# Kernel tuning notes

Hardware: AMD Instinct MI355X
Metric: run time of the kernel (lower is better)

The kernel has to match this reference:

```python
import jax, jax.numpy as jnp
import numpy as np

N = 50000
E = 640000
M = 400000
D_IN, H1, H2, H3, D_OUT = 256, 128, 128, 64, 32


def _glorot(key, shape, gain=1.0):
    fan_in, fan_out = shape[0], shape[1]
    lim = gain * np.sqrt(6.0 / (fan_in + fan_out))
    return jax.random.uniform(key, shape, jnp.float32, -lim, lim)


def setup_inputs() -> dict:
    key = jax.random.key(0)
    ks = jax.random.split(key, 16)
    x = jax.random.normal(ks[0], (N, D_IN), jnp.float32)
    edge_index = jax.random.randint(ks[1], (2, E), 0, N, jnp.int64)
    train_sample = jax.random.randint(ks[2], (M, 2), 0, N, jnp.int64)
    g = 1.414
    return {
        "x": x,
        "edge_index": edge_index,
        "train_sample": train_sample,
        "W1": _glorot(ks[3], (D_IN, H1)),
        "W2": _glorot(ks[4], (H1, H2)),
        "tf_w1": _glorot(ks[5], (H2, H3), g), "tf_b1": jnp.zeros((H3,), jnp.float32),
        "tf_w2": _glorot(ks[6], (H3, D_OUT), g), "tf_b2": jnp.zeros((D_OUT,), jnp.float32),
        "tg_w1": _glorot(ks[7], (H2, H3), g), "tg_b1": jnp.zeros((H3,), jnp.float32),
        "tg_w2": _glorot(ks[8], (H3, D_OUT), g), "tg_b2": jnp.zeros((D_OUT,), jnp.float32),
    }


def _gcn_conv(x, W, src, dst, norm, n):
    # GCNConv (no bias): out = D^-1/2 (A+I) D^-1/2 (x @ W)
    h = x @ W
    msg = h[src] * norm[:, None]          # [E+N, H]
    return jax.ops.segment_sum(msg, dst, num_segments=n)


def reference(x, edge_index, train_sample, W1, W2, tf_w1, tf_b1, tf_w2, tf_b2, tg_w1, tg_b1, tg_w2, tg_b2):
    n = x.shape[0]
    loop = jnp.arange(n, dtype=edge_index.dtype)
    src = jnp.concatenate([edge_index[0], loop])
    dst = jnp.concatenate([edge_index[1], loop])
    deg = jnp.zeros((n,), x.dtype).at[dst].add(1.0)
    dis = jax.lax.rsqrt(deg)              # deg >= 1 due to self loops
    norm = dis[src] * dis[dst]

    # encode
    h = jax.nn.elu(_gcn_conv(x, W1, src, dst, norm, n))
    embed = _gcn_conv(h, W2, src, dst, norm, n)

    # tf / target MLP branches (dropout p=0.01 treated as identity)
    lrelu = jax.nn.leaky_relu
    tf = lrelu(lrelu(embed @ tf_w1 + tf_b1) @ tf_w2 + tf_b2)
    tg = lrelu(lrelu(embed @ tg_w1 + tg_b1) @ tg_w2 + tg_b2)

    # gather + dot decode
    t = tf[train_sample[:, 0]]
    u = tg[train_sample[:, 1]]
    return jnp.sum(t * u, axis=1, keepdims=True)  # [M,1]
```

## Files before the change

### kernel.cpp

```cpp
#include <hip/hip_runtime.h>
#include <hip/hip_bf16.h>
#include <math.h>


typedef __attribute__((ext_vector_type(8))) short short8v;
typedef __attribute__((ext_vector_type(4))) float f32x4;
typedef __attribute__((ext_vector_type(4))) _Float16 half4v;

__device__ inline unsigned short f2bf_rne(float f) {
    unsigned u = __float_as_uint(f);
    unsigned r = u + 0x7FFFu + ((u >> 16) & 1u);
    return (unsigned short)(r >> 16);
}
__device__ inline float bf2f(unsigned short h) {
    return __uint_as_float(((unsigned)h) << 16);
}

__global__ void zero_ideg_kernel(int* __restrict__ ideg, int n) {
    int i = blockIdx.x * 256 + threadIdx.x;
    if (i < n) ideg[i] = 0;
}

__global__ void ideg_accum_kernel(int* __restrict__ ideg, const int* __restrict__ dst, int e) {
    int i = blockIdx.x * 256 + threadIdx.x;
    if (i < e) atomicAdd(&ideg[dst[i]], 1);
}

__global__ __launch_bounds__(256) void scan_blk_kernel(const int* __restrict__ ideg,
                                                       int* __restrict__ row_ptr,
                                                       float* __restrict__ dis,
                                                       int* __restrict__ partials, int n) {
    __shared__ int wsum[4];
    const int t = threadIdx.x;
    const int lane = t & 63;
    const int wid = t >> 6;
    const int i0 = blockIdx.x * 1024 + t * 4;
    int4 v = make_int4(0, 0, 0, 0);
    if (i0 + 3 < n) {
        v = *(const int4*)&ideg[i0];
    } else if (i0 < n) {
        v.x = ideg[i0];
        if (i0 + 1 < n) v.y = ideg[i0 + 1];
        if (i0 + 2 < n) v.z = ideg[i0 + 2];
    }
    if (i0 < n) {
        dis[i0] = rsqrtf(1.f + (float)v.x);
        if (i0 + 1 < n) dis[i0 + 1] = rsqrtf(1.f + (float)v.y);
        if (i0 + 2 < n) dis[i0 + 2] = rsqrtf(1.f + (float)v.z);
        if (i0 + 3 < n) dis[i0 + 3] = rsqrtf(1.f + (float)v.w);
    }
    int s = v.x + v.y + v.z + v.w;
    int incl = s;
#pragma unroll
    for (int off = 1; off < 64; off <<= 1) {
        int tv = __shfl_up(incl, off, 64);
        if (lane >= off) incl += tv;
    }
    if (lane == 63) wsum[wid] = incl;
    __syncthreads();
    if (t == 0) {
        int a = 0;
#pragma unroll
        for (int ww = 0; ww < 4; ++ww) { int tmp = wsum[ww]; wsum[ww] = a; a += tmp; }
    }
    __syncthreads();
    int ex = wsum[wid] + incl - s;
    if (i0 < n) {
        row_ptr[i0] = ex;
        if (i0 + 1 < n) row_ptr[i0 + 1] = ex + v.x;
        if (i0 + 2 < n) row_ptr[i0 + 2] = ex + v.x + v.y;
        if (i0 + 3 < n) row_ptr[i0 + 3] = ex + v.x + v.y + v.z;
    }
    if (t == 255) partials[blockIdx.x] = wsum[3] + incl;
}

__global__ void scan_part_kernel(int* __restrict__ partials, int nb) {
    int lane = threadIdx.x;
    int v = (lane < nb) ? partials[lane] : 0;
    int incl = v;
#pragma unroll
    for (int off = 1; off < 64; off <<= 1) {
        int tv = __shfl_up(incl, off, 64);
        if (lane >= off) incl += tv;
    }
    if (lane < nb) partials[lane] = incl - v;
}

__global__ void scan_add_kernel(int* __restrict__ row_ptr, const int* __restrict__ partials, int n) {
    int i = blockIdx.x * 256 + threadIdx.x;
    if (i < n) row_ptr[i] += partials[i >> 10];
}

__global__ void fill_kernel(const int* __restrict__ src, const int* __restrict__ dst,
                            int* __restrict__ row_ptr, int* __restrict__ csr, int e) {
    int i = blockIdx.x * 256 + threadIdx.x;
    if (i < e) {
        int d = dst[i];
        int pos = atomicAdd(&row_ptr[d], 1);
        csr[pos] = src[i];
    }
}

__global__ void prep_weights_kernel(
    const float* __restrict__ W1, const float* __restrict__ W2,
    const float* __restrict__ tfw1, const float* __restrict__ tfb1,
    const float* __restrict__ tfw2, const float* __restrict__ tfb2,
    const float* __restrict__ tgw1, const float* __restrict__ tgb1,
    const float* __restrict__ tgw2, const float* __restrict__ tgb2,
    unsigned short* __restrict__ wf,
    float* __restrict__ bcat1, float* __restrict__ bcat2)
{
    int id = blockIdx.x * 256 + threadIdx.x;
    if (id >= 147456) {
        if (id < 147456 + 128) {
            int c = id - 147456;
            bcat1[c] = (c < 64) ? tfb1[c] : tgb1[c - 64];
        } else if (id < 147456 + 192) {
            int c = id - 147456 - 128;
            bcat2[c] = (c < 32) ? tfb2[c] : tgb2[c - 32];
        }
        return;
    }
    int base, NF;
    int lid;
    if (id < 65536)       { base = 0;      NF = 8; lid = id; }
    else if (id < 98304)  { base = 65536;  NF = 8; lid = id - 65536; }
    else if (id < 131072) { base = 98304;  NF = 8; lid = id - 98304; }
    else                  { base = 131072; NF = 4; lid = id - 131072; }

    int j    = lid & 7;
    int lane = (lid >> 3) & 63;
    int h    = (lid >> 9) & 1;
    int rest = lid >> 10;
    int c    = rest % NF;
    int kk   = rest / NF;
    int k    = kk * 32 + (lane >> 4) * 8 + j;
    int col  = c * 16 + (lane & 15);

    float w;
    if (id < 65536) {
        w = W1[k * 128 + col];
    } else if (id < 98304) {
        w = W2[k * 128 + col];
    } else if (id < 131072) {
        w = (col < 64) ? tfw1[k * 64 + col] : tgw1[k * 64 + (col - 64)];
    } else {
        w = 0.f;
        if (k < 64 && col < 32) w = tfw2[k * 32 + col];
        else if (k >= 64 && col >= 32) w = tgw2[(k - 64) * 32 + (col - 32)];
    }
    unsigned short hb = f2bf_rne(w);
    wf[base + lid] = h ? f2bf_rne(w - bf2f(hb)) : hb;
}

template <int K, int NCOL, bool ELU_IN, bool LRELU, bool BIAS, bool OUT_HALF>
__global__ __launch_bounds__(256) void mfma_gemm_kernel(
    const float* __restrict__ X, const unsigned short* __restrict__ wf,
    const float* __restrict__ bias, void* __restrict__ Yv, int nrows)
{
    constexpr int NF = NCOL / 16;
    constexpr int NK = K / 32;

    const int t = threadIdx.x;
    const int lane = t & 63;
    const int w = t >> 6;
    const int row0 = blockIdx.x * 64 + w * 16;

    const int arow = row0 + (lane & 15);
    const bool rowok = arow < nrows;
    const float* xrow = X + (size_t)arow * K + ((lane >> 4) * 8);

    f32x4 acc[NF];
#pragma unroll
    for (int c = 0; c < NF; ++c) acc[c] = (f32x4){0.f, 0.f, 0.f, 0.f};

#pragma unroll 2
    for (int kk = 0; kk < NK; ++kk) {
        float4 v0 = make_float4(0.f, 0.f, 0.f, 0.f);
        float4 v1 = v0;
        if (rowok) {
            v0 = *(const float4*)&xrow[kk * 32];
            v1 = *(const float4*)&xrow[kk * 32 + 4];
        }
        if (ELU_IN) {
            v0.x = (v0.x > 0.f) ? v0.x : expm1f(v0.x);
            v0.y = (v0.y > 0.f) ? v0.y : expm1f(v0.y);
            v0.z = (v0.z > 0.f) ? v0.z : expm1f(v0.z);
            v0.w = (v0.w > 0.f) ? v0.w : expm1f(v0.w);
            v1.x = (v1.x > 0.f) ? v1.x : expm1f(v1.x);
            v1.y = (v1.y > 0.f) ? v1.y : expm1f(v1.y);
            v1.z = (v1.z > 0.f) ? v1.z : expm1f(v1.z);
            v1.w = (v1.w > 0.f) ? v1.w : expm1f(v1.w);
        }
        float a[8] = {v0.x, v0.y, v0.z, v0.w, v1.x, v1.y, v1.z, v1.w};
        short8v ah, al;
#pragma unroll
        for (int j = 0; j < 8; ++j) {
            unsigned short hb = f2bf_rne(a[j]);
            ah[j] = (short)hb;
            al[j] = (short)f2bf_rne(a[j] - bf2f(hb));
        }
        const unsigned short* wfk = wf + (size_t)(kk * NF * 2) * 512 + lane * 8;
        short8v bh[NF], bl[NF];
#pragma unroll
        for (int c = 0; c < NF; ++c) {
            bh[c] = *(const short8v*)(wfk + (c * 2 + 0) * 512);
            bl[c] = *(const short8v*)(wfk + (c * 2 + 1) * 512);
        }
#pragma unroll
        for (int c = 0; c < NF; ++c) {
            acc[c] = __builtin_amdgcn_mfma_f32_16x16x32_bf16(ah, bh[c], acc[c], 0, 0, 0);
            acc[c] = __builtin_amdgcn_mfma_f32_16x16x32_bf16(al, bh[c], acc[c], 0, 0, 0);
            acc[c] = __builtin_amdgcn_mfma_f32_16x16x32_bf16(ah, bl[c], acc[c], 0, 0, 0);
        }
    }

#pragma unroll
    for (int c = 0; c < NF; ++c) {
        int gcol = c * 16 + (lane & 15);
        float bv = BIAS ? bias[gcol] : 0.f;
#pragma unroll
        for (int q = 0; q < 4; ++q) {
            int grow = row0 + (lane >> 4) * 4 + q;
            if (grow < nrows) {
                float o = acc[c][q] + bv;
                if (LRELU) o = (o > 0.f) ? o : 0.01f * o;
                if (OUT_HALF) ((_Float16*)Yv)[(size_t)grow * NCOL + gcol] = (_Float16)o;
                else          ((float*)Yv)[(size_t)grow * NCOL + gcol] = o;
            }
        }
    }
}

__global__ __launch_bounds__(256) void fused_heads_kernel(
    const float* __restrict__ X, const unsigned short* __restrict__ h1f,
    const unsigned short* __restrict__ h2f, const float* __restrict__ bcat1,
    const float* __restrict__ bcat2, _Float16* __restrict__ Z, int nrows)
{
    constexpr int LDT = 136;
    __shared__ unsigned short t1h[4][16][LDT];
    __shared__ unsigned short t1l[4][16][LDT];

    const int t = threadIdx.x;
    const int lane = t & 63;
    const int w = t >> 6;
    const int row0 = blockIdx.x * 64 + w * 16;

    const int arow = row0 + (lane & 15);
    const bool rowok = arow < nrows;
    const float* xrow = X + (size_t)arow * 128 + ((lane >> 4) * 8);

    f32x4 acc[8];
#pragma unroll
    for (int c = 0; c < 8; ++c) acc[c] = (f32x4){0.f, 0.f, 0.f, 0.f};

#pragma unroll 2
    for (int kk = 0; kk < 4; ++kk) {
        float4 v0 = make_float4(0.f, 0.f, 0.f, 0.f);
        float4 v1 = v0;
        if (rowok) {
            v0 = *(const float4*)&xrow[kk * 32];
            v1 = *(const float4*)&xrow[kk * 32 + 4];
        }
        float a[8] = {v0.x, v0.y, v0.z, v0.w, v1.x, v1.y, v1.z, v1.w};
        short8v ah, al;
#pragma unroll
        for (int j = 0; j < 8; ++j) {
            unsigned short hb = f2bf_rne(a[j]);
            ah[j] = (short)hb;
            al[j] = (short)f2bf_rne(a[j] - bf2f(hb));
        }
        const unsigned short* wfk = h1f + (size_t)(kk * 16) * 512 + lane * 8;
        short8v bh[8], bl[8];
#pragma unroll
        for (int c = 0; c < 8; ++c) {
            bh[c] = *(const short8v*)(wfk + (c * 2 + 0) * 512);
            bl[c] = *(const short8v*)(wfk + (c * 2 + 1) * 512);
        }
#pragma unroll
        for (int c = 0; c < 8; ++c) {
            acc[c] = __builtin_amdgcn_mfma_f32_16x16x32_bf16(ah, bh[c], acc[c], 0, 0, 0);
            acc[c] = __builtin_amdgcn_mfma_f32_16x16x32_bf16(al, bh[c], acc[c], 0, 0, 0);
            acc[c] = __builtin_amdgcn_mfma_f32_16x16x32_bf16(ah, bl[c], acc[c], 0, 0, 0);
        }
    }

#pragma unroll
    for (int c = 0; c < 8; ++c) {
        int col = c * 16 + (lane & 15);
        float bv = bcat1[col];
#pragma unroll
        for (int q = 0; q < 4; ++q) {
            int r = (lane >> 4) * 4 + q;
            float o = acc[c][q] + bv;
            o = (o > 0.f) ? o : 0.01f * o;
            unsigned short hb = f2bf_rne(o);
            t1h[w][r][col] = hb;
            t1l[w][r][col] = f2bf_rne(o - bf2f(hb));
        }
    }

    f32x4 acc2[4];
#pragma unroll
    for (int c = 0; c < 4; ++c) acc2[c] = (f32x4){0.f, 0.f, 0.f, 0.f};

#pragma unroll
    for (int kk = 0; kk < 4; ++kk) {
        int koff = kk * 32 + (lane >> 4) * 8;
        short8v ah = *(const short8v*)&t1h[w][lane & 15][koff];
        short8v al = *(const short8v*)&t1l[w][lane & 15][koff];
        const unsigned short* wfk = h2f + (size_t)(kk * 8) * 512 + lane * 8;
#pragma unroll
        for (int c = 0; c < 4; ++c) {
            short8v bh = *(const short8v*)(wfk + (c * 2 + 0) * 512);
            short8v bl = *(const short8v*)(wfk + (c * 2 + 1) * 512);
            acc2[c] = __builtin_amdgcn_mfma_f32_16x16x32_bf16(ah, bh, acc2[c], 0, 0, 0);
            acc2[c] = __builtin_amdgcn_mfma_f32_16x16x32_bf16(al, bh, acc2[c], 0, 0, 0);
            acc2[c] = __builtin_amdgcn_mfma_f32_16x16x32_bf16(ah, bl, acc2[c], 0, 0, 0);
        }
    }

#pragma unroll
    for (int c = 0; c < 4; ++c) {
        int gcol = c * 16 + (lane & 15);
        float bv = bcat2[gcol];
#pragma unroll
        for (int q = 0; q < 4; ++q) {
            int grow = row0 + (lane >> 4) * 4 + q;
            if (grow < nrows) {
                float o = acc2[c][q] + bv;
                o = (o > 0.f) ? o : 0.01f * o;
                Z[(size_t)grow * 64 + gcol] = (_Float16)o;
            }
        }
    }
}

__global__ __launch_bounds__(256) void gather_kernel(const _Float16* __restrict__ h,
                                                     const int* __restrict__ row_ptr,
                                                     const int* __restrict__ csr,
                                                     const float* __restrict__ dis,
                                                     float* __restrict__ outp, int n) {
    int node = blockIdx.x * 8 + (threadIdx.x >> 5);
    int l = threadIdx.x & 31;
    if (node >= n) return;
    int beg = (node == 0) ? 0 : row_ptr[node - 1];
    int end = row_ptr[node];
    float dd = dis[node];
    const half4v* h4 = (const half4v*)h;
    half4v self = h4[(size_t)node * 32 + l];
    float ax = (float)self[0] * dd, ay = (float)self[1] * dd;
    float az = (float)self[2] * dd, aw = (float)self[3] * dd;
    int j = beg;
    for (; j + 4 <= end; j += 4) {
        int s0 = csr[j + 0], s1 = csr[j + 1], s2 = csr[j + 2], s3 = csr[j + 3];
        float d0 = dis[s0], d1 = dis[s1], d2 = dis[s2], d3 = dis[s3];
        half4v v0 = h4[(size_t)s0 * 32 + l];
        half4v v1 = h4[(size_t)s1 * 32 + l];
        half4v v2 = h4[(size_t)s2 * 32 + l];
        half4v v3 = h4[(size_t)s3 * 32 + l];
        ax += (float)v0[0] * d0 + (float)v1[0] * d1 + (float)v2[0] * d2 + (float)v3[0] * d3;
        ay += (float)v0[1] * d0 + (float)v1[1] * d1 + (float)v2[1] * d2 + (float)v3[1] * d3;
        az += (float)v0[2] * d0 + (float)v1[2] * d1 + (float)v2[2] * d2 + (float)v3[2] * d3;
        aw += (float)v0[3] * d0 + (float)v1[3] * d1 + (float)v2[3] * d2 + (float)v3[3] * d3;
    }
    for (; j < end; ++j) {
        int s = csr[j];
        float ds = dis[s];
        half4v v = h4[(size_t)s * 32 + l];
        ax += (float)v[0] * ds; ay += (float)v[1] * ds;
        az += (float)v[2] * ds; aw += (float)v[3] * ds;
    }
    float4 o;
    o.x = ax * dd; o.y = ay * dd; o.z = az * dd; o.w = aw * dd;
    ((float4*)outp)[(size_t)node * 32 + l] = o;
}

__global__ void dot_kernel(const _Float16* __restrict__ Z,
                           const int* __restrict__ ts, float* __restrict__ out, int m) {
    int gid = blockIdx.x * 256 + threadIdx.x;
    int s = gid >> 3;
    int l = gid & 7;
    if (s >= m) return;
    int ti = ts[2 * s + 0];
    int ui = ts[2 * s + 1];
    const half4v* Z4 = (const half4v*)Z;
    half4v a = Z4[(size_t)ti * 16 + l];
    half4v b = Z4[(size_t)ui * 16 + 8 + l];
    float d = (float)a[0] * (float)b[0] + (float)a[1] * (float)b[1]
            + (float)a[2] * (float)b[2] + (float)a[3] * (float)b[3];
    d += __shfl_down(d, 4, 8);
    d += __shfl_down(d, 2, 8);
    d += __shfl_down(d, 1, 8);
    if (l == 0) out[s] = d;
}

extern "C" void kernel_launch(void* const* d_in, const int* in_sizes, int n_in,
                              void* d_out, int out_size, void* d_ws, size_t ws_size,
                              hipStream_t stream) {
    const float* x     = (const float*)d_in[0];
    const int*   ei    = (const int*)d_in[1];
    const int*   ts    = (const int*)d_in[2];
    const float* W1    = (const float*)d_in[3];
    const float* W2    = (const float*)d_in[4];
    const float* tf_w1 = (const float*)d_in[5];
    const float* tf_b1 = (const float*)d_in[6];
    const float* tf_w2 = (const float*)d_in[7];
    const float* tf_b2 = (const float*)d_in[8];
    const float* tg_w1 = (const float*)d_in[9];
    const float* tg_b1 = (const float*)d_in[10];
    const float* tg_w2 = (const float*)d_in[11];
    const float* tg_b2 = (const float*)d_in[12];
    float* out = (float*)d_out;

    const int n = in_sizes[0] / 256;
    const int e = in_sizes[1] / 2;
    const int m = in_sizes[2] / 2;
    const int* src = ei;
    const int* dstp = ei + e;

    float* wsf = (float*)d_ws;
    float* dis     = wsf;
    int*   row_ptr = (int*)(wsf + 50176);
    int*   partials = row_ptr + 50048;
    int*   ideg    = (int*)(wsf + 100352);
    int*   csr     = (int*)(wsf + 100352);
    unsigned short* wfrag = (unsigned short*)(wsf + 740416);
    unsigned short* w1f = wfrag;
    unsigned short* w2f = wfrag + 65536;
    unsigned short* h1f = wfrag + 98304;
    unsigned short* h2f = wfrag + 131072;
    float* bcat1 = wsf + 740416 + 73728;
    float* bcat2 = wsf + 814272;
    float* A = wsf + 814336;
    float* B = A + (size_t)n * 128;
    float* C = B + (size_t)n * 128;
    _Float16* A16 = (_Float16*)A;
    _Float16* C16 = (_Float16*)C;
    _Float16* Z16 = (_Float16*)C;

    const int nb_n = (n + 255) / 256;
    const int nb_e = (e + 255) / 256;
    const int nsb  = (n + 1023) / 1024;
    const int gg   = (n + 7) / 8;
    const int gm   = (n + 63) / 64;

    zero_ideg_kernel<<<nb_n, 256, 0, stream>>>(ideg, n);
    ideg_accum_kernel<<<nb_e, 256, 0, stream>>>(ideg, dstp, e);
    scan_blk_kernel<<<nsb, 256, 0, stream>>>(ideg, row_ptr, dis, partials, n);
    scan_part_kernel<<<1, 64, 0, stream>>>(partials, nsb);
    scan_add_kernel<<<nb_n, 256, 0, stream>>>(row_ptr, partials, n);
    fill_kernel<<<nb_e, 256, 0, stream>>>(src, dstp, row_ptr, csr, e);

    prep_weights_kernel<<<(147648 + 255) / 256, 256, 0, stream>>>(
        W1, W2, tf_w1, tf_b1, tf_w2, tf_b2, tg_w1, tg_b1, tg_w2, tg_b2,
        wfrag, bcat1, bcat2);

    mfma_gemm_kernel<256, 128, false, false, false, true><<<gm, 256, 0, stream>>>(x, w1f, nullptr, A16, n);
    gather_kernel<<<gg, 256, 0, stream>>>(A16, row_ptr, csr, dis, B, n);

    mfma_gemm_kernel<128, 128, true, false, false, true><<<gm, 256, 0, stream>>>(B, w2f, nullptr, C16, n);
    gather_kernel<<<gg, 256, 0, stream>>>(C16, row_ptr, csr, dis, A, n);

    fused_heads_kernel<<<gm, 256, 0, stream>>>(A, h1f, h2f, bcat1, bcat2, Z16, n);

    dot_kernel<<<(m * 8 + 255) / 256, 256, 0, stream>>>(Z16, ts, out, m);
}
```

Before: 304.4 us.

## Fuse neighbor gather into following GEMM via shared-memory tile

The separate gather kernels, which wrote fp32 aggregated features to global memory, are removed. The aggregation is now done per block into an fp16 LDS tile, which the next MFMA GEMM (layer 2, or the fused heads) reads directly, with ELU applied during the gather. This drops two kernel launches and the fp32 round trip of the intermediate features. In exchange, each wave gathers its 16 rows serially at lower parallelism per node, the intermediate tiles are held at fp16 rather than split hi/lo precision, and extra block syncs are added.

```diff
diff --git a/kernel.cpp b/kernel.cpp
--- a/kernel.cpp
+++ b/kernel.cpp
@@ -6,6 +6,7 @@
 typedef __attribute__((ext_vector_type(8))) short short8v;
 typedef __attribute__((ext_vector_type(4))) float f32x4;
 typedef __attribute__((ext_vector_type(4))) _Float16 half4v;
+typedef __attribute__((ext_vector_type(8))) _Float16 half8v;
 
 __device__ inline unsigned short f2bf_rne(float f) {
     unsigned u = __float_as_uint(f);
@@ -153,10 +154,10 @@
     wf[base + lid] = h ? f2bf_rne(w - bf2f(hb)) : hb;
 }
 
-template <int K, int NCOL, bool ELU_IN, bool LRELU, bool BIAS, bool OUT_HALF>
+template <int K, int NCOL>
 __global__ __launch_bounds__(256) void mfma_gemm_kernel(
     const float* __restrict__ X, const unsigned short* __restrict__ wf,
-    const float* __restrict__ bias, void* __restrict__ Yv, int nrows)
+    _Float16* __restrict__ Y, int nrows)
 {
     constexpr int NF = NCOL / 16;
     constexpr int NK = K / 32;
@@ -182,16 +183,6 @@
             v0 = *(const float4*)&xrow[kk * 32];
             v1 = *(const float4*)&xrow[kk * 32 + 4];
         }
-        if (ELU_IN) {
-            v0.x = (v0.x > 0.f) ? v0.x : expm1f(v0.x);
-            v0.y = (v0.y > 0.f) ? v0.y : expm1f(v0.y);
-            v0.z = (v0.z > 0.f) ? v0.z : expm1f(v0.z);
-            v0.w = (v0.w > 0.f) ? v0.w : expm1f(v0.w);
-            v1.x = (v1.x > 0.f) ? v1.x : expm1f(v1.x);
-            v1.y = (v1.y > 0.f) ? v1.y : expm1f(v1.y);
-            v1.z = (v1.z > 0.f) ? v1.z : expm1f(v1.z);
-            v1.w = (v1.w > 0.f) ? v1.w : expm1f(v1.w);
-        }
         float a[8] = {v0.x, v0.y, v0.z, v0.w, v1.x, v1.y, v1.z, v1.w};
         short8v ah, al;
 #pragma unroll
@@ -218,72 +209,161 @@
 #pragma unroll
     for (int c = 0; c < NF; ++c) {
         int gcol = c * 16 + (lane & 15);
-        float bv = BIAS ? bias[gcol] : 0.f;
 #pragma unroll
         for (int q = 0; q < 4; ++q) {
             int grow = row0 + (lane >> 4) * 4 + q;
-            if (grow < nrows) {
-                float o = acc[c][q] + bv;
-                if (LRELU) o = (o > 0.f) ? o : 0.01f * o;
-                if (OUT_HALF) ((_Float16*)Yv)[(size_t)grow * NCOL + gcol] = (_Float16)o;
-                else          ((float*)Yv)[(size_t)grow * NCOL + gcol] = o;
+            if (grow < nrows) Y[(size_t)grow * NCOL + gcol] = (_Float16)acc[c][q];
+        }
+    }
+}
+
+template <bool ELU>
+__device__ inline void gather_to_lds(const _Float16* __restrict__ hsrc,
+                                     const int* __restrict__ row_ptr,
+                                     const int* __restrict__ csr,
+                                     const float* __restrict__ dis,
+                                     _Float16 (*gtile)[136],
+                                     int row0, int lane, int n) {
+    const half4v* h4 = (const half4v*)hsrc;
+    const int l = lane & 31;
+    for (int p = 0; p < 8; ++p) {
+        int lr = p * 2 + (lane >> 5);
+        int node = row0 + lr;
+        float ax = 0.f, ay = 0.f, az = 0.f, aw = 0.f;
+        if (node < n) {
+            int beg = (node == 0) ? 0 : row_ptr[node - 1];
+            int end = row_ptr[node];
+            float dd = dis[node];
+            half4v self = h4[(size_t)node * 32 + l];
+            ax = (float)self[0] * dd; ay = (float)self[1] * dd;
+            az = (float)self[2] * dd; aw = (float)self[3] * dd;
+            int j = beg;
+            for (; j + 4 <= end; j += 4) {
+                int s0 = csr[j + 0], s1 = csr[j + 1], s2 = csr[j + 2], s3 = csr[j + 3];
+                float d0 = dis[s0], d1 = dis[s1], d2 = dis[s2], d3 = dis[s3];
+                half4v v0 = h4[(size_t)s0 * 32 + l];
+                half4v v1 = h4[(size_t)s1 * 32 + l];
+                half4v v2 = h4[(size_t)s2 * 32 + l];
+                half4v v3 = h4[(size_t)s3 * 32 + l];
+                ax += (float)v0[0] * d0 + (float)v1[0] * d1 + (float)v2[0] * d2 + (float)v3[0] * d3;
+                ay += (float)v0[1] * d0 + (float)v1[1] * d1 + (float)v2[1] * d2 + (float)v3[1] * d3;
+                az += (float)v0[2] * d0 + (float)v1[2] * d1 + (float)v2[2] * d2 + (float)v3[2] * d3;
+                aw += (float)v0[3] * d0 + (float)v1[3] * d1 + (float)v2[3] * d2 + (float)v3[3] * d3;
             }
-        }
-    }
-}
-
-__global__ __launch_bounds__(256) void fused_heads_kernel(
-    const float* __restrict__ X, const unsigned short* __restrict__ h1f,
-    const unsigned short* __restrict__ h2f, const float* __restrict__ bcat1,
-    const float* __restrict__ bcat2, _Float16* __restrict__ Z, int nrows)
+            for (; j < end; ++j) {
+                int s = csr[j];
+                float ds = dis[s];
+                half4v v = h4[(size_t)s * 32 + l];
+                ax += (float)v[0] * ds; ay += (float)v[1] * ds;
+                az += (float)v[2] * ds; aw += (float)v[3] * ds;
+            }
+            ax *= dd; ay *= dd; az *= dd; aw *= dd;
+            if (ELU) {
+                ax = (ax > 0.f) ? ax : expm1f(ax);
+                ay = (ay > 0.f) ? ay : expm1f(ay);
+                az = (az > 0.f) ? az : expm1f(az);
+                aw = (aw > 0.f) ? aw : expm1f(aw);
+            }
+        }
+        half4v o;
+        o[0] = (_Float16)ax; o[1] = (_Float16)ay; o[2] = (_Float16)az; o[3] = (_Float16)aw;
+        *(half4v*)&gtile[lr][l * 4] = o;
+    }
+}
+
+__global__ __launch_bounds__(256, 6) void fused_gather_gemm_kernel(
+    const _Float16* __restrict__ hsrc, const int* __restrict__ row_ptr,
+    const int* __restrict__ csr, const float* __restrict__ dis,
+    const unsigned short* __restrict__ wf, _Float16* __restrict__ Y, int n)
 {
-    constexpr int LDT = 136;
-    __shared__ unsigned short t1h[4][16][LDT];
-    __shared__ unsigned short t1l[4][16][LDT];
-
+    __shared__ _Float16 gtile[4][16][136];
     const int t = threadIdx.x;
     const int lane = t & 63;
     const int w = t >> 6;
     const int row0 = blockIdx.x * 64 + w * 16;
 
-    const int arow = row0 + (lane & 15);
-    const bool rowok = arow < nrows;
-    const float* xrow = X + (size_t)arow * 128 + ((lane >> 4) * 8);
+    gather_to_lds<true>(hsrc, row_ptr, csr, dis, gtile[w], row0, lane, n);
+    __syncthreads();
 
     f32x4 acc[8];
 #pragma unroll
     for (int c = 0; c < 8; ++c) acc[c] = (f32x4){0.f, 0.f, 0.f, 0.f};
 
-#pragma unroll 2
+#pragma unroll
     for (int kk = 0; kk < 4; ++kk) {
-        float4 v0 = make_float4(0.f, 0.f, 0.f, 0.f);
-        float4 v1 = v0;
-        if (rowok) {
-            v0 = *(const float4*)&xrow[kk * 32];
-            v1 = *(const float4*)&xrow[kk * 32 + 4];
-        }
-        float a[8] = {v0.x, v0.y, v0.z, v0.w, v1.x, v1.y, v1.z, v1.w};
+        half8v av = *(const half8v*)&gtile[w][lane & 15][kk * 32 + (lane >> 4) * 8];
         short8v ah, al;
 #pragma unroll
         for (int j = 0; j < 8; ++j) {
-            unsigned short hb = f2bf_rne(a[j]);
+            float f = (float)av[j];
+            unsigned short hb = f2bf_rne(f);
             ah[j] = (short)hb;
-            al[j] = (short)f2bf_rne(a[j] - bf2f(hb));
+            al[j] = (short)f2bf_rne(f - bf2f(hb));
+        }
+        const unsigned short* wfk = wf + (size_t)(kk * 16) * 512 + lane * 8;
+#pragma unroll
+        for (int c = 0; c < 8; ++c) {
+            short8v bh = *(const short8v*)(wfk + (c * 2 + 0) * 512);
+            short8v bl = *(const short8v*)(wfk + (c * 2 + 1) * 512);
+            acc[c] = __builtin_amdgcn_mfma_f32_16x16x32_bf16(ah, bh, acc[c], 0, 0, 0);
+            acc[c] = __builtin_amdgcn_mfma_f32_16x16x32_bf16(al, bh, acc[c], 0, 0, 0);
+            acc[c] = __builtin_amdgcn_mfma_f32_16x16x32_bf16(ah, bl, acc[c], 0, 0, 0);
+        }
+    }
+
+#pragma unroll
+    for (int c = 0; c < 8; ++c) {
+        int gcol = c * 16 + (lane & 15);
+#pragma unroll
+        for (int q = 0; q < 4; ++q) {
+            int grow = row0 + (lane >> 4) * 4 + q;
+            if (grow < n) Y[(size_t)grow * 128 + gcol] = (_Float16)acc[c][q];
+        }
+    }
+}
+
+__global__ __launch_bounds__(256, 6) void fused_gather_heads_kernel(
+    const _Float16* __restrict__ hsrc, const int* __restrict__ row_ptr,
+    const int* __restrict__ csr, const float* __restrict__ dis,
+    const unsigned short* __restrict__ h1f, const unsigned short* __restrict__ h2f,
+    const float* __restrict__ bcat1, const float* __restrict__ bcat2,
+    _Float16* __restrict__ Z, int n)
+{
+    __shared__ _Float16 gtile[4][16][136];
+    const int t = threadIdx.x;
+    const int lane = t & 63;
+    const int w = t >> 6;
+    const int row0 = blockIdx.x * 64 + w * 16;
+
+    gather_to_lds<false>(hsrc, row_ptr, csr, dis, gtile[w], row0, lane, n);
+    __syncthreads();
+
+    f32x4 acc[8];
+#pragma unroll
+    for (int c = 0; c < 8; ++c) acc[c] = (f32x4){0.f, 0.f, 0.f, 0.f};
+
+#pragma unroll
+    for (int kk = 0; kk < 4; ++kk) {
+        half8v av = *(const half8v*)&gtile[w][lane & 15][kk * 32 + (lane >> 4) * 8];
+        short8v ah, al;
+#pragma unroll
+        for (int j = 0; j < 8; ++j) {
+            float f = (float)av[j];
+            unsigned short hb = f2bf_rne(f);
+            ah[j] = (short)hb;
+            al[j] = (short)f2bf_rne(f - bf2f(hb));
         }
         const unsigned short* wfk = h1f + (size_t)(kk * 16) * 512 + lane * 8;
-        short8v bh[8], bl[8];
 #pragma unroll
         for (int c = 0; c < 8; ++c) {
-            bh[c] = *(const short8v*)(wfk + (c * 2 + 0) * 512);
-            bl[c] = *(const short8v*)(wfk + (c * 2 + 1) * 512);
-        }
-#pragma unroll
-        for (int c = 0; c < 8; ++c) {
-            acc[c] = __builtin_amdgcn_mfma_f32_16x16x32_bf16(ah, bh[c], acc[c], 0, 0, 0);
-            acc[c] = __builtin_amdgcn_mfma_f32_16x16x32_bf16(al, bh[c], acc[c], 0, 0, 0);
-            acc[c] = __builtin_amdgcn_mfma_f32_16x16x32_bf16(ah, bl[c], acc[c], 0, 0, 0);
-        }
-    }
+            short8v bh = *(const short8v*)(wfk + (c * 2 + 0) * 512);
+            short8v bl = *(const short8v*)(wfk + (c * 2 + 1) * 512);
+            acc[c] = __builtin_amdgcn_mfma_f32_16x16x32_bf16(ah, bh, acc[c], 0, 0, 0);
+            acc[c] = __builtin_amdgcn_mfma_f32_16x16x32_bf16(al, bh, acc[c], 0, 0, 0);
+            acc[c] = __builtin_amdgcn_mfma_f32_16x16x32_bf16(ah, bl, acc[c], 0, 0, 0);
+        }
+    }
+    __syncthreads();
 
 #pragma unroll
     for (int c = 0; c < 8; ++c) {
@@ -294,11 +374,10 @@
             int r = (lane >> 4) * 4 + q;
             float o = acc[c][q] + bv;
             o = (o > 0.f) ? o : 0.01f * o;
-            unsigned short hb = f2bf_rne(o);
-            t1h[w][r][col] = hb;
-            t1l[w][r][col] = f2bf_rne(o - bf2f(hb));
-        }
-    }
+            gtile[w][r][col] = (_Float16)o;
+        }
+    }
+    __syncthreads();
 
     f32x4 acc2[4];
 #pragma unroll
@@ -306,9 +385,15 @@
 
 #pragma unroll
     for (int kk = 0; kk < 4; ++kk) {
-        int koff = kk * 32 + (lane >> 4) * 8;
-        short8v ah = *(const short8v*)&t1h[w][lane & 15][koff];
-        short8v al = *(const short8v*)&t1l[w][lane & 15][koff];
+        half8v av = *(const half8v*)&gtile[w][lane & 15][kk * 32 + (lane >> 4) * 8];
+        short8v ah, al;
+#pragma unroll
+        for (int j = 0; j < 8; ++j) {
+            float f = (float)av[j];
+            unsigned short hb = f2bf_rne(f);
+            ah[j] = (short)hb;
+            al[j] = (short)f2bf_rne(f - bf2f(hb));
+        }
         const unsigned short* wfk = h2f + (size_t)(kk * 8) * 512 + lane * 8;
 #pragma unroll
         for (int c = 0; c < 4; ++c) {
@@ -327,53 +412,13 @@
 #pragma unroll
         for (int q = 0; q < 4; ++q) {
             int grow = row0 + (lane >> 4) * 4 + q;
-            if (grow < nrows) {
+            if (grow < n) {
                 float o = acc2[c][q] + bv;
                 o = (o > 0.f) ? o : 0.01f * o;
                 Z[(size_t)grow * 64 + gcol] = (_Float16)o;
             }
         }
     }
-}
-
-__global__ __launch_bounds__(256) void gather_kernel(const _Float16* __restrict__ h,
-                                                     const int* __restrict__ row_ptr,
-                                                     const int* __restrict__ csr,
-                                                     const float* __restrict__ dis,
-                                                     float* __restrict__ outp, int n) {
-    int node = blockIdx.x * 8 + (threadIdx.x >> 5);
-    int l = threadIdx.x & 31;
-    if (node >= n) return;
-    int beg = (node == 0) ? 0 : row_ptr[node - 1];
-    int end = row_ptr[node];
-    float dd = dis[node];
-    const half4v* h4 = (const half4v*)h;
-    half4v self = h4[(size_t)node * 32 + l];
-    float ax = (float)self[0] * dd, ay = (float)self[1] * dd;
-    float az = (float)self[2] * dd, aw = (float)self[3] * dd;
-    int j = beg;
-    for (; j + 4 <= end; j += 4) {
-        int s0 = csr[j + 0], s1 = csr[j + 1], s2 = csr[j + 2], s3 = csr[j + 3];
-        float d0 = dis[s0], d1 = dis[s1], d2 = dis[s2], d3 = dis[s3];
-        half4v v0 = h4[(size_t)s0 * 32 + l];
-        half4v v1 = h4[(size_t)s1 * 32 + l];
-        half4v v2 = h4[(size_t)s2 * 32 + l];
-        half4v v3 = h4[(size_t)s3 * 32 + l];
-        ax += (float)v0[0] * d0 + (float)v1[0] * d1 + (float)v2[0] * d2 + (float)v3[0] * d3;
-        ay += (float)v0[1] * d0 + (float)v1[1] * d1 + (float)v2[1] * d2 + (float)v3[1] * d3;
-        az += (float)v0[2] * d0 + (float)v1[2] * d1 + (float)v2[2] * d2 + (float)v3[2] * d3;
-        aw += (float)v0[3] * d0 + (float)v1[3] * d1 + (float)v2[3] * d2 + (float)v3[3] * d3;
-    }
-    for (; j < end; ++j) {
-        int s = csr[j];
-        float ds = dis[s];
-        half4v v = h4[(size_t)s * 32 + l];
-        ax += (float)v[0] * ds; ay += (float)v[1] * ds;
-        az += (float)v[2] * ds; aw += (float)v[3] * ds;
-    }
-    float4 o;
-    o.x = ax * dd; o.y = ay * dd; o.z = az * dd; o.w = aw * dd;
-    ((float4*)outp)[(size_t)node * 32 + l] = o;
 }
 
 __global__ void dot_kernel(const _Float16* __restrict__ Z,
@@ -437,12 +482,11 @@
     float* C = B + (size_t)n * 128;
     _Float16* A16 = (_Float16*)A;
     _Float16* C16 = (_Float16*)C;
-    _Float16* Z16 = (_Float16*)C;
+    _Float16* Z16 = (_Float16*)B;
 
     const int nb_n = (n + 255) / 256;
     const int nb_e = (e + 255) / 256;
     const int nsb  = (n + 1023) / 1024;
-    const int gg   = (n + 7) / 8;
     const int gm   = (n + 63) / 64;
 
     zero_ideg_kernel<<<nb_n, 256, 0, stream>>>(ideg, n);
@@ -456,13 +500,12 @@
         W1, W2, tf_w1, tf_b1, tf_w2, tf_b2, tg_w1, tg_b1, tg_w2, tg_b2,
         wfrag, bcat1, bcat2);
 
-    mfma_gemm_kernel<256, 128, false, false, false, true><<<gm, 256, 0, stream>>>(x, w1f, nullptr, A16, n);
-    gather_kernel<<<gg, 256, 0, stream>>>(A16, row_ptr, csr, dis, B, n);
-
-    mfma_gemm_kernel<128, 128, true, false, false, true><<<gm, 256, 0, stream>>>(B, w2f, nullptr, C16, n);
-    gather_kernel<<<gg, 256, 0, stream>>>(C16, row_ptr, csr, dis, A, n);
-
-    fused_heads_kernel<<<gm, 256, 0, stream>>>(A, h1f, h2f, bcat1, bcat2, Z16, n);
+    mfma_gemm_kernel<256, 128><<<gm, 256, 0, stream>>>(x, w1f, A16, n);
+
+    fused_gather_gemm_kernel<<<gm, 256, 0, stream>>>(A16, row_ptr, csr, dis, w2f, C16, n);
+
+    fused_gather_heads_kernel<<<gm, 256, 0, stream>>>(
+        C16, row_ptr, csr, dis, h1f, h2f, bcat1, bcat2, Z16, n);
 
     dot_kernel<<<(m * 8 + 255) / 256, 256, 0, stream>>>(Z16, ts, out, m);
 }
```

Measured after the change: 322.2 us. 5.9% more time.
